# Kernel tuning notes

Hardware: AMD Instinct MI355X
Metric: run time of the kernel (lower is better)

## Reference

```python
import jax, jax.numpy as jnp
import numpy as np

THRESHOLD = 0.4


def _pair_feat(xs, xd):
    # pair_mode='both': [src, dst, |src-dst|, src*dst] along feature axis
    return jnp.concatenate([xs, xd, jnp.abs(xs - xd), xs * xd], axis=-1)


def _mlp(pf, W1, b1, W2, b2):
    h = jax.nn.relu(pf @ W1 + b1)
    return (h @ W2 + b2)[..., 0]


def setup_inputs() -> dict:
    key = jax.random.key(0)
    k1, k2, k3, k4, k5 = jax.random.split(key, 5)
    N, F, E, H = 1024, 64, 65536, 32
    x = jax.random.normal(k1, (N, F), dtype=jnp.float32)
    edge_index = jax.random.randint(k2, (2, E), 0, N, dtype=jnp.int64)
    edge_index_global = jax.random.randint(k3, (2, E), 0, N, dtype=jnp.int64)
    W1 = jax.random.normal(k4, (4 * F, H), dtype=jnp.float32) * (1.0 / np.sqrt(4 * F))
    b1 = jnp.zeros((H,), dtype=jnp.float32)
    W2 = jax.random.normal(k5, (H, 1), dtype=jnp.float32) * (1.0 / np.sqrt(H))
    b2 = jnp.zeros((1,), dtype=jnp.float32)
    return {"x": x, "edge_index": edge_index, "edge_index_global": edge_index_global,
            "W1": W1, "b1": b1, "W2": W2, "b2": b2}


def reference(x, edge_index, edge_index_global, W1, b1, W2, b2):
    # ---- sparse edge branch ----
    xs = x[edge_index[0]]            # [E, F]
    xd = x[edge_index[1]]            # [E, F]
    pf = _pair_feat(xs, xd)          # [E, 4F]
    edge_logits = _mlp(pf, W1, b1, W2, b2)        # [E]
    edge_probs = jax.nn.sigmoid(edge_logits)      # [E]
    edge_actions = (edge_probs > THRESHOLD).astype(x.dtype)  # [E]
    # (new_edge_index / raw_edge_index in the original are data-dependent
    #  boolean selections of edge columns; the mask is edge_actions==1.)

    # ---- dense all-pairs branch (train=True) ----
    N, F = x.shape
    xi = jnp.broadcast_to(x[:, None, :], (N, N, F))  # src of pair (i,j)
    xj = jnp.broadcast_to(x[None, :, :], (N, N, F))  # dst of pair (i,j)
    pf_all = _pair_feat(xi, xj)                      # [N, N, 4F] -- dominant intermediate
    logits_all = _mlp(pf_all, W1, b1, W2, b2)        # [N, N]
    P = jax.nn.sigmoid(logits_all)                   # [N, N]

    return edge_probs, edge_actions, P
```

## Files before the change

kernel.cpp:

```cpp
#include <hip/hip_runtime.h>
#include <hip/hip_bf16.h>
#include <math.h>

#define NN 1024
#define FD 64
#define EE 65536
#define HD 32

typedef __attribute__((ext_vector_type(8))) short short8;
typedef __attribute__((ext_vector_type(4))) float floatx4;

__device__ __forceinline__ float sigmoid_f(float z) {
  return 1.0f / (1.0f + expf(-z));
}
__device__ __forceinline__ float sigmoid_fast(float z) {
  return 1.0f / (1.0f + __expf(-z));
}

__device__ __forceinline__ unsigned pack_bf16_trunc(float hi, float lo) {
  unsigned a = __builtin_bit_cast(unsigned, hi);
  unsigned b = __builtin_bit_cast(unsigned, lo);
  return __builtin_amdgcn_perm(a, b, 0x07060302u);
}

__device__ __forceinline__ short8 pack8(const float* v) {
  union { unsigned u[4]; short8 s; } p;
#pragma unroll
  for (int t = 0; t < 4; ++t) p.u[t] = pack_bf16_trunc(v[2 * t + 1], v[2 * t]);
  return p.s;
}

struct Frag3 { short8 a0, a1, a2; };

__device__ __forceinline__ Frag3 split_pack(const float* v) {
  float r[8], r2[8];
#pragma unroll
  for (int t = 0; t < 8; ++t) {
    const unsigned uv = __builtin_bit_cast(unsigned, v[t]);
    const float f0 = __builtin_bit_cast(float, uv & 0xFFFF0000u);
    const float rr = v[t] - f0;
    const unsigned ur = __builtin_bit_cast(unsigned, rr);
    const float f1 = __builtin_bit_cast(float, ur & 0xFFFF0000u);
    r[t] = rr;
    r2[t] = rr - f1;
  }
  Frag3 f;
  f.a0 = pack8(v);
  f.a1 = pack8(r);
  f.a2 = pack8(r2);
  return f;
}

__global__ __launch_bounds__(256) void pre_kernel3(
    const float* __restrict__ x, const float* __restrict__ W1,
    const float* __restrict__ b1, float* __restrict__ pre,
    short* __restrict__ Wt0, short* __restrict__ Wt1, short* __restrict__ Wt2) {
  const int blk = blockIdx.x;
  const int t = threadIdx.x;
  if (blk < 256) {
    const int node = blk * 4 + (t >> 6);
    const int which = (t >> 5) & 1;
    const int h = t & 31;
    const float* xr = x + node * FD;
    const float* wp = W1 + which * FD * HD + h;
    float acc = which ? 0.0f : b1[h];
#pragma unroll
    for (int f = 0; f < FD; ++f) acc = fmaf(xr[f], wp[f * HD], acc);
    pre[which * (NN * HD) + node * HD + h] = acc;
  } else {
    for (int idx = t; idx < 32 * 128; idx += 256) {
      const int h = idx >> 7;
      const int k = idx & 127;
      const int f = k & 63;
      const int b = 2 + (k >> 6);
      const float v = W1[(b * FD + f) * HD + h];
      const unsigned uv = __builtin_bit_cast(unsigned, v);
      const unsigned u0 = uv & 0xFFFF0000u;
      const float f0 = __builtin_bit_cast(float, u0);
      const float r = v - f0;
      const unsigned u1 = __builtin_bit_cast(unsigned, r) & 0xFFFF0000u;
      const float f1 = __builtin_bit_cast(float, u1);
      const float r2 = r - f1;
      const unsigned u2 = __builtin_bit_cast(unsigned, r2) & 0xFFFF0000u;
      Wt0[idx] = (short)(u0 >> 16);
      Wt1[idx] = (short)(u1 >> 16);
      Wt2[idx] = (short)(u2 >> 16);
    }
  }
}

__device__ __forceinline__ void edge_chunk(
    const float* feat, const short* __restrict__ Wt0,
    const short* __restrict__ Wt1, const short* __restrict__ Wt2,
    int c, int q, int kc, floatx4& acc0, floatx4& acc1) {
  const Frag3 A = split_pack(feat);
  const int off0 = c * 128 + kc * 32 + q * 8;
  const int off1 = (16 + c) * 128 + kc * 32 + q * 8;
  const short8 B00 = *(const short8*)(Wt0 + off0);
  const short8 B01 = *(const short8*)(Wt1 + off0);
  const short8 B02 = *(const short8*)(Wt2 + off0);
  const short8 B10 = *(const short8*)(Wt0 + off1);
  const short8 B11 = *(const short8*)(Wt1 + off1);
  const short8 B12 = *(const short8*)(Wt2 + off1);
  acc0 = __builtin_amdgcn_mfma_f32_16x16x32_bf16(A.a0, B00, acc0, 0, 0, 0);
  acc0 = __builtin_amdgcn_mfma_f32_16x16x32_bf16(A.a0, B01, acc0, 0, 0, 0);
  acc0 = __builtin_amdgcn_mfma_f32_16x16x32_bf16(A.a0, B02, acc0, 0, 0, 0);
  acc0 = __builtin_amdgcn_mfma_f32_16x16x32_bf16(A.a1, B00, acc0, 0, 0, 0);
  acc0 = __builtin_amdgcn_mfma_f32_16x16x32_bf16(A.a1, B01, acc0, 0, 0, 0);
  acc0 = __builtin_amdgcn_mfma_f32_16x16x32_bf16(A.a2, B00, acc0, 0, 0, 0);
  acc1 = __builtin_amdgcn_mfma_f32_16x16x32_bf16(A.a0, B10, acc1, 0, 0, 0);
  acc1 = __builtin_amdgcn_mfma_f32_16x16x32_bf16(A.a0, B11, acc1, 0, 0, 0);
  acc1 = __builtin_amdgcn_mfma_f32_16x16x32_bf16(A.a0, B12, acc1, 0, 0, 0);
  acc1 = __builtin_amdgcn_mfma_f32_16x16x32_bf16(A.a1, B10, acc1, 0, 0, 0);
  acc1 = __builtin_amdgcn_mfma_f32_16x16x32_bf16(A.a1, B11, acc1, 0, 0, 0);
  acc1 = __builtin_amdgcn_mfma_f32_16x16x32_bf16(A.a2, B10, acc1, 0, 0, 0);
}

__global__ __launch_bounds__(256, 2) void edge_mfma_kernel(
    const float* __restrict__ x, const int* __restrict__ eidx,
    const float* __restrict__ pre, const short* __restrict__ Wt0,
    const short* __restrict__ Wt1, const short* __restrict__ Wt2,
    const float* __restrict__ W2, const float* __restrict__ b2,
    float* __restrict__ out) {
  const int lane = threadIdx.x & 63;
  const int q = lane >> 4;
  const int c = lane & 15;
  const int e0 = (blockIdx.x * 4 + (threadIdx.x >> 6)) * 16;

  const bool is64 = (eidx[1] == 0) && (eidx[3] == 0) && (eidx[5] == 0);
  int s_c, d_c;
  if (is64) {
    s_c = eidx[2 * (e0 + c)];
    d_c = eidx[2 * (EE + e0 + c)];
  } else {
    s_c = eidx[e0 + c];
    d_c = eidx[EE + e0 + c];
  }
  const float* xs = x + (size_t)s_c * FD;
  const float* xd = x + (size_t)d_c * FD;

  floatx4 acc0, acc1;
#pragma unroll
  for (int r = 0; r < 4; ++r) {
    const int m = q * 4 + r;
    const int sm = __shfl(s_c, m);
    const int dm = __shfl(d_c, m);
    acc0[r] = pre[sm * HD + c] + pre[NN * HD + dm * HD + c];
    acc1[r] = pre[sm * HD + 16 + c] + pre[NN * HD + dm * HD + 16 + c];
  }

  {
    const floatx4 s0 = *(const floatx4*)(xs + q * 8);
    const floatx4 s1 = *(const floatx4*)(xs + q * 8 + 4);
    const floatx4 d0 = *(const floatx4*)(xd + q * 8);
    const floatx4 d1 = *(const floatx4*)(xd + q * 8 + 4);
    float ad[8], pr[8];
#pragma unroll
    for (int t = 0; t < 4; ++t) {
      ad[t] = fabsf(s0[t] - d0[t]);     pr[t] = s0[t] * d0[t];
      ad[4 + t] = fabsf(s1[t] - d1[t]); pr[4 + t] = s1[t] * d1[t];
    }
    edge_chunk(ad, Wt0, Wt1, Wt2, c, q, 0, acc0, acc1);
    edge_chunk(pr, Wt0, Wt1, Wt2, c, q, 2, acc0, acc1);
  }
  {
    const floatx4 s0 = *(const floatx4*)(xs + 32 + q * 8);
    const floatx4 s1 = *(const floatx4*)(xs + 32 + q * 8 + 4);
    const floatx4 d0 = *(const floatx4*)(xd + 32 + q * 8);
    const floatx4 d1 = *(const floatx4*)(xd + 32 + q * 8 + 4);
    float ad[8], pr[8];
#pragma unroll
    for (int t = 0; t < 4; ++t) {
      ad[t] = fabsf(s0[t] - d0[t]);     pr[t] = s0[t] * d0[t];
      ad[4 + t] = fabsf(s1[t] - d1[t]); pr[4 + t] = s1[t] * d1[t];
    }
    edge_chunk(ad, Wt0, Wt1, Wt2, c, q, 1, acc0, acc1);
    edge_chunk(pr, Wt0, Wt1, Wt2, c, q, 3, acc0, acc1);
  }

  const float w2a = W2[c], w2b = W2[16 + c];
  const float b2v = b2[0];
  float tr[4];
#pragma unroll
  for (int r = 0; r < 4; ++r) {
    tr[r] = fmaxf(acc0[r], 0.0f) * w2a;
    tr[r] = fmaf(fmaxf(acc1[r], 0.0f), w2b, tr[r]);
#pragma unroll
    for (int m = 1; m <= 8; m <<= 1) tr[r] += __shfl_xor(tr[r], m);
  }
  float zs = tr[0];
  zs = (c == 1) ? tr[1] : zs;
  zs = (c == 2) ? tr[2] : zs;
  zs = (c == 3) ? tr[3] : zs;
  if (c < 4) {
    const int e = e0 + q * 4 + c;
    const float z = zs + b2v;
    out[e] = sigmoid_f(z);
    out[EE + e] = (z > -0.40546510810816444f) ? 1.0f : 0.0f;
  }
}

__global__ __launch_bounds__(256, 2) void dense_mfma_kernel(
    const float* __restrict__ x, const float* __restrict__ pre,
    const short* __restrict__ Wt0, const float* __restrict__ W2,
    const float* __restrict__ b2, float* __restrict__ outP) {
  const int lane = threadIdx.x & 63;
  const int w = threadIdx.x >> 6;
  const int q = lane >> 4;
  const int c = lane & 15;
  const int j0 = blockIdx.x * 64 + w * 16;
  const int i0 = blockIdx.y * 16;

  short8 Bf[2][4];
#pragma unroll
  for (int n = 0; n < 2; ++n)
#pragma unroll
    for (int s = 0; s < 4; ++s)
      Bf[n][s] = *(const short8*)(Wt0 + (n * 16 + c) * 128 + s * 32 + q * 8);

  const float* xj = x + (size_t)(j0 + c) * FD;
  float jA[8], jB[8];
#pragma unroll
  for (int t = 0; t < 4; ++t) {
    jA[t] = xj[q * 8 + t];      jA[4 + t] = xj[q * 8 + 4 + t];
    jB[t] = xj[32 + q * 8 + t]; jB[4 + t] = xj[32 + q * 8 + 4 + t];
  }

  float pdA[4], pdB[4];
#pragma unroll
  for (int r = 0; r < 4; ++r) {
    pdA[r] = pre[NN * HD + (j0 + q * 4 + r) * HD + c];
    pdB[r] = pre[NN * HD + (j0 + q * 4 + r) * HD + 16 + c];
  }
  const float w2a = W2[c], w2b = W2[16 + c];
  const float b2v = b2[0];

  for (int i = i0; i < i0 + 16; ++i) {
    const float* xi = x + (size_t)i * FD;
    const float psa = pre[i * HD + c];
    const float psb = pre[i * HD + 16 + c];
    floatx4 acc0, acc1;
#pragma unroll
    for (int r = 0; r < 4; ++r) {
      acc0[r] = psa + pdA[r];
      acc1[r] = psb + pdB[r];
    }
    {
      const floatx4 i0v = *(const floatx4*)(xi + q * 8);
      const floatx4 i1v = *(const floatx4*)(xi + q * 8 + 4);
      float ad[8], pr[8];
#pragma unroll
      for (int t = 0; t < 4; ++t) {
        ad[t] = fabsf(i0v[t] - jA[t]);         pr[t] = i0v[t] * jA[t];
        ad[4 + t] = fabsf(i1v[t] - jA[4 + t]); pr[4 + t] = i1v[t] * jA[4 + t];
      }
      const short8 fad = pack8(ad);
      const short8 fpr = pack8(pr);
      acc0 = __builtin_amdgcn_mfma_f32_16x16x32_bf16(fad, Bf[0][0], acc0, 0, 0, 0);
      acc1 = __builtin_amdgcn_mfma_f32_16x16x32_bf16(fad, Bf[1][0], acc1, 0, 0, 0);
      acc0 = __builtin_amdgcn_mfma_f32_16x16x32_bf16(fpr, Bf[0][2], acc0, 0, 0, 0);
      acc1 = __builtin_amdgcn_mfma_f32_16x16x32_bf16(fpr, Bf[1][2], acc1, 0, 0, 0);
    }
    {
      const floatx4 i0v = *(const floatx4*)(xi + 32 + q * 8);
      const floatx4 i1v = *(const floatx4*)(xi + 32 + q * 8 + 4);
      float ad[8], pr[8];
#pragma unroll
      for (int t = 0; t < 4; ++t) {
        ad[t] = fabsf(i0v[t] - jB[t]);         pr[t] = i0v[t] * jB[t];
        ad[4 + t] = fabsf(i1v[t] - jB[4 + t]); pr[4 + t] = i1v[t] * jB[4 + t];
      }
      const short8 fad = pack8(ad);
      const short8 fpr = pack8(pr);
      acc0 = __builtin_amdgcn_mfma_f32_16x16x32_bf16(fad, Bf[0][1], acc0, 0, 0, 0);
      acc1 = __builtin_amdgcn_mfma_f32_16x16x32_bf16(fad, Bf[1][1], acc1, 0, 0, 0);
      acc0 = __builtin_amdgcn_mfma_f32_16x16x32_bf16(fpr, Bf[0][3], acc0, 0, 0, 0);
      acc1 = __builtin_amdgcn_mfma_f32_16x16x32_bf16(fpr, Bf[1][3], acc1, 0, 0, 0);
    }
    float tr[4];
#pragma unroll
    for (int r = 0; r < 4; ++r) {
      tr[r] = fmaxf(acc0[r], 0.0f) * w2a;
      tr[r] = fmaf(fmaxf(acc1[r], 0.0f), w2b, tr[r]);
#pragma unroll
      for (int m = 1; m <= 8; m <<= 1) tr[r] += __shfl_xor(tr[r], m);
    }
    float zs = tr[0];
    zs = (c == 1) ? tr[1] : zs;
    zs = (c == 2) ? tr[2] : zs;
    zs = (c == 3) ? tr[3] : zs;
    if (c < 4) {
      outP[(size_t)i * NN + j0 + q * 4 + c] = sigmoid_fast(zs + b2v);
    }
  }
}

__device__ __forceinline__ float pair_logit_full(
    const float* __restrict__ xs, const float* __restrict__ xd,
    const float* __restrict__ W1, const float* __restrict__ b1,
    const float* __restrict__ W2, const float b2v) {
  float acc[HD];
#pragma unroll
  for (int h = 0; h < HD; ++h) acc[h] = b1[h];
#pragma unroll 1
  for (int f = 0; f < FD; ++f) {
    const float a = xs[f], b = xd[f];
    const float ad = fabsf(a - b), pr = a * b;
#pragma unroll
    for (int h = 0; h < HD; ++h) {
      float t0 = fmaf(a, W1[f * HD + h], acc[h]);
      t0 = fmaf(b, W1[(FD + f) * HD + h], t0);
      t0 = fmaf(ad, W1[(2 * FD + f) * HD + h], t0);
      acc[h] = fmaf(pr, W1[(3 * FD + f) * HD + h], t0);
    }
  }
  float z = b2v;
#pragma unroll
  for (int h = 0; h < HD; ++h) z = fmaf(fmaxf(acc[h], 0.0f), W2[h], z);
  return z;
}

__global__ __launch_bounds__(256) void edge_kernel_fb(
    const float* __restrict__ x, const int* __restrict__ eidx,
    const float* __restrict__ W1, const float* __restrict__ b1,
    const float* __restrict__ W2, const float* __restrict__ b2,
    float* __restrict__ out) {
  const int e = blockIdx.x * 256 + threadIdx.x;
  const bool is64 = (eidx[1] == 0) && (eidx[3] == 0) && (eidx[5] == 0);
  int s, d;
  if (is64) { s = eidx[2 * e]; d = eidx[2 * (EE + e)]; }
  else { s = eidx[e]; d = eidx[EE + e]; }
  const float z = pair_logit_full(x + (size_t)s * FD, x + (size_t)d * FD,
                                  W1, b1, W2, b2[0]);
  const float p = sigmoid_f(z);
  out[e] = p;
  out[EE + e] = (p > 0.4f) ? 1.0f : 0.0f;
}

__global__ __launch_bounds__(256) void dense_full_fb(
    const float* __restrict__ x, const float* __restrict__ W1,
    const float* __restrict__ b1, const float* __restrict__ W2,
    const float* __restrict__ b2, float* __restrict__ outP) {
  const int j = blockIdx.x * 64 + threadIdx.x % 64;
  const int i = blockIdx.y * 4 + threadIdx.x / 64;
  const float z = pair_logit_full(x + (size_t)i * FD, x + (size_t)j * FD,
                                  W1, b1, W2, b2[0]);
  outP[(size_t)i * NN + j] = sigmoid_f(z);
}

extern "C" void kernel_launch(void* const* d_in, const int* in_sizes, int n_in,
                              void* d_out, int out_size, void* d_ws, size_t ws_size,
                              hipStream_t stream) {
  const float* x  = (const float*)d_in[0];
  const int*  ei  = (const int*)d_in[1];
  const float* W1 = (const float*)d_in[3];
  const float* b1 = (const float*)d_in[4];
  const float* W2 = (const float*)d_in[5];
  const float* b2 = (const float*)d_in[6];
  float* out  = (float*)d_out;
  float* outP = out + 2 * EE;

  const size_t pre_bytes = (size_t)2 * NN * HD * sizeof(float);
  const size_t wt_elems = 32 * 128;
  const size_t need = pre_bytes + 3 * wt_elems * sizeof(short);
  if (ws_size >= need) {
    float* pre = (float*)d_ws;
    short* Wt0 = (short*)((char*)d_ws + pre_bytes);
    short* Wt1 = Wt0 + wt_elems;
    short* Wt2 = Wt1 + wt_elems;
    pre_kernel3<<<257, 256, 0, stream>>>(x, W1, b1, pre, Wt0, Wt1, Wt2);
    edge_mfma_kernel<<<1024, 256, 0, stream>>>(x, ei, pre, Wt0, Wt1, Wt2,
                                               W2, b2, out);
    dense_mfma_kernel<<<dim3(16, 64), 256, 0, stream>>>(x, pre, Wt0, W2, b2,
                                                        outP);
  } else {
    edge_kernel_fb<<<EE / 256, 256, 0, stream>>>(x, ei, W1, b1, W2, b2, out);
    dense_full_fb<<<dim3(NN / 64, NN / 4), 256, 0, stream>>>(
        x, W1, b1, W2, b2, outP);
  }
}
```

Before: 110.8 us.

## Transpose MFMA operands so hidden dim lies on rows, cutting shuffle reductions

Swaps the A and B operands of the bf16 MFMAs in both the edge and dense kernels, so each lane's accumulator holds four hidden units of a single edge or pair instead of four edges for one hidden unit. The W2 dot product then reduces mostly in registers and needs only two cross-lane shuffles instead of sixteen. The bias terms and W2 can be loaded as float4 vectors. Occupancy hints are raised and the small precompute dot product is split into four independent accumulators to shorten its dependency chain. The hint changes risk register spills.

```diff
diff --git a/kernel.cpp b/kernel.cpp
--- a/kernel.cpp
+++ b/kernel.cpp
@@ -63,10 +63,15 @@
     const int h = t & 31;
     const float* xr = x + node * FD;
     const float* wp = W1 + which * FD * HD + h;
-    float acc = which ? 0.0f : b1[h];
-#pragma unroll
-    for (int f = 0; f < FD; ++f) acc = fmaf(xr[f], wp[f * HD], acc);
-    pre[which * (NN * HD) + node * HD + h] = acc;
+    float a0 = which ? 0.0f : b1[h], a1 = 0.0f, a2 = 0.0f, a3 = 0.0f;
+#pragma unroll
+    for (int f = 0; f < FD; f += 4) {
+      a0 = fmaf(xr[f + 0], wp[(f + 0) * HD], a0);
+      a1 = fmaf(xr[f + 1], wp[(f + 1) * HD], a1);
+      a2 = fmaf(xr[f + 2], wp[(f + 2) * HD], a2);
+      a3 = fmaf(xr[f + 3], wp[(f + 3) * HD], a3);
+    }
+    pre[which * (NN * HD) + node * HD + h] = (a0 + a1) + (a2 + a3);
   } else {
     for (int idx = t; idx < 32 * 128; idx += 256) {
       const int h = idx >> 7;
@@ -93,30 +98,30 @@
     const float* feat, const short* __restrict__ Wt0,
     const short* __restrict__ Wt1, const short* __restrict__ Wt2,
     int c, int q, int kc, floatx4& acc0, floatx4& acc1) {
-  const Frag3 A = split_pack(feat);
+  const Frag3 B = split_pack(feat);
   const int off0 = c * 128 + kc * 32 + q * 8;
   const int off1 = (16 + c) * 128 + kc * 32 + q * 8;
-  const short8 B00 = *(const short8*)(Wt0 + off0);
-  const short8 B01 = *(const short8*)(Wt1 + off0);
-  const short8 B02 = *(const short8*)(Wt2 + off0);
-  const short8 B10 = *(const short8*)(Wt0 + off1);
-  const short8 B11 = *(const short8*)(Wt1 + off1);
-  const short8 B12 = *(const short8*)(Wt2 + off1);
-  acc0 = __builtin_amdgcn_mfma_f32_16x16x32_bf16(A.a0, B00, acc0, 0, 0, 0);
-  acc0 = __builtin_amdgcn_mfma_f32_16x16x32_bf16(A.a0, B01, acc0, 0, 0, 0);
-  acc0 = __builtin_amdgcn_mfma_f32_16x16x32_bf16(A.a0, B02, acc0, 0, 0, 0);
-  acc0 = __builtin_amdgcn_mfma_f32_16x16x32_bf16(A.a1, B00, acc0, 0, 0, 0);
-  acc0 = __builtin_amdgcn_mfma_f32_16x16x32_bf16(A.a1, B01, acc0, 0, 0, 0);
-  acc0 = __builtin_amdgcn_mfma_f32_16x16x32_bf16(A.a2, B00, acc0, 0, 0, 0);
-  acc1 = __builtin_amdgcn_mfma_f32_16x16x32_bf16(A.a0, B10, acc1, 0, 0, 0);
-  acc1 = __builtin_amdgcn_mfma_f32_16x16x32_bf16(A.a0, B11, acc1, 0, 0, 0);
-  acc1 = __builtin_amdgcn_mfma_f32_16x16x32_bf16(A.a0, B12, acc1, 0, 0, 0);
-  acc1 = __builtin_amdgcn_mfma_f32_16x16x32_bf16(A.a1, B10, acc1, 0, 0, 0);
-  acc1 = __builtin_amdgcn_mfma_f32_16x16x32_bf16(A.a1, B11, acc1, 0, 0, 0);
-  acc1 = __builtin_amdgcn_mfma_f32_16x16x32_bf16(A.a2, B10, acc1, 0, 0, 0);
-}
-
-__global__ __launch_bounds__(256, 2) void edge_mfma_kernel(
+  const short8 A00 = *(const short8*)(Wt0 + off0);
+  const short8 A01 = *(const short8*)(Wt1 + off0);
+  const short8 A02 = *(const short8*)(Wt2 + off0);
+  const short8 A10 = *(const short8*)(Wt0 + off1);
+  const short8 A11 = *(const short8*)(Wt1 + off1);
+  const short8 A12 = *(const short8*)(Wt2 + off1);
+  acc0 = __builtin_amdgcn_mfma_f32_16x16x32_bf16(A00, B.a0, acc0, 0, 0, 0);
+  acc0 = __builtin_amdgcn_mfma_f32_16x16x32_bf16(A01, B.a0, acc0, 0, 0, 0);
+  acc0 = __builtin_amdgcn_mfma_f32_16x16x32_bf16(A02, B.a0, acc0, 0, 0, 0);
+  acc0 = __builtin_amdgcn_mfma_f32_16x16x32_bf16(A00, B.a1, acc0, 0, 0, 0);
+  acc0 = __builtin_amdgcn_mfma_f32_16x16x32_bf16(A01, B.a1, acc0, 0, 0, 0);
+  acc0 = __builtin_amdgcn_mfma_f32_16x16x32_bf16(A00, B.a2, acc0, 0, 0, 0);
+  acc1 = __builtin_amdgcn_mfma_f32_16x16x32_bf16(A10, B.a0, acc1, 0, 0, 0);
+  acc1 = __builtin_amdgcn_mfma_f32_16x16x32_bf16(A11, B.a0, acc1, 0, 0, 0);
+  acc1 = __builtin_amdgcn_mfma_f32_16x16x32_bf16(A12, B.a0, acc1, 0, 0, 0);
+  acc1 = __builtin_amdgcn_mfma_f32_16x16x32_bf16(A10, B.a1, acc1, 0, 0, 0);
+  acc1 = __builtin_amdgcn_mfma_f32_16x16x32_bf16(A11, B.a1, acc1, 0, 0, 0);
+  acc1 = __builtin_amdgcn_mfma_f32_16x16x32_bf16(A10, B.a2, acc1, 0, 0, 0);
+}
+
+__global__ __launch_bounds__(256, 3) void edge_mfma_kernel(
     const float* __restrict__ x, const int* __restrict__ eidx,
     const float* __restrict__ pre, const short* __restrict__ Wt0,
     const short* __restrict__ Wt1, const short* __restrict__ Wt2,
@@ -140,13 +145,16 @@
   const float* xd = x + (size_t)d_c * FD;
 
   floatx4 acc0, acc1;
-#pragma unroll
-  for (int r = 0; r < 4; ++r) {
-    const int m = q * 4 + r;
-    const int sm = __shfl(s_c, m);
-    const int dm = __shfl(d_c, m);
-    acc0[r] = pre[sm * HD + c] + pre[NN * HD + dm * HD + c];
-    acc1[r] = pre[sm * HD + 16 + c] + pre[NN * HD + dm * HD + 16 + c];
+  {
+    const floatx4 psA = *(const floatx4*)(pre + s_c * HD + q * 4);
+    const floatx4 psB = *(const floatx4*)(pre + s_c * HD + 16 + q * 4);
+    const floatx4 pdA = *(const floatx4*)(pre + NN * HD + d_c * HD + q * 4);
+    const floatx4 pdB = *(const floatx4*)(pre + NN * HD + d_c * HD + 16 + q * 4);
+#pragma unroll
+    for (int r = 0; r < 4; ++r) {
+      acc0[r] = psA[r] + pdA[r];
+      acc1[r] = psB[r] + pdB[r];
+    }
   }
 
   {
@@ -178,29 +186,25 @@
     edge_chunk(pr, Wt0, Wt1, Wt2, c, q, 3, acc0, acc1);
   }
 
-  const float w2a = W2[c], w2b = W2[16 + c];
-  const float b2v = b2[0];
-  float tr[4];
+  const floatx4 w2A = *(const floatx4*)(W2 + q * 4);
+  const floatx4 w2B = *(const floatx4*)(W2 + 16 + q * 4);
+  float tv = 0.0f;
 #pragma unroll
   for (int r = 0; r < 4; ++r) {
-    tr[r] = fmaxf(acc0[r], 0.0f) * w2a;
-    tr[r] = fmaf(fmaxf(acc1[r], 0.0f), w2b, tr[r]);
-#pragma unroll
-    for (int m = 1; m <= 8; m <<= 1) tr[r] += __shfl_xor(tr[r], m);
-  }
-  float zs = tr[0];
-  zs = (c == 1) ? tr[1] : zs;
-  zs = (c == 2) ? tr[2] : zs;
-  zs = (c == 3) ? tr[3] : zs;
-  if (c < 4) {
-    const int e = e0 + q * 4 + c;
-    const float z = zs + b2v;
+    tv = fmaf(fmaxf(acc0[r], 0.0f), w2A[r], tv);
+    tv = fmaf(fmaxf(acc1[r], 0.0f), w2B[r], tv);
+  }
+  tv += __shfl_xor(tv, 16);
+  tv += __shfl_xor(tv, 32);
+  if (lane < 16) {
+    const int e = e0 + lane;
+    const float z = tv + b2[0];
     out[e] = sigmoid_f(z);
     out[EE + e] = (z > -0.40546510810816444f) ? 1.0f : 0.0f;
   }
 }
 
-__global__ __launch_bounds__(256, 2) void dense_mfma_kernel(
+__global__ __launch_bounds__(256, 4) void dense_mfma_kernel(
     const float* __restrict__ x, const float* __restrict__ pre,
     const short* __restrict__ Wt0, const float* __restrict__ W2,
     const float* __restrict__ b2, float* __restrict__ outP) {
@@ -211,12 +215,12 @@
   const int j0 = blockIdx.x * 64 + w * 16;
   const int i0 = blockIdx.y * 16;
 
-  short8 Bf[2][4];
+  short8 Af[2][4];
 #pragma unroll
   for (int n = 0; n < 2; ++n)
 #pragma unroll
     for (int s = 0; s < 4; ++s)
-      Bf[n][s] = *(const short8*)(Wt0 + (n * 16 + c) * 128 + s * 32 + q * 8);
+      Af[n][s] = *(const short8*)(Wt0 + (n * 16 + c) * 128 + s * 32 + q * 8);
 
   const float* xj = x + (size_t)(j0 + c) * FD;
   float jA[8], jB[8];
@@ -226,24 +230,21 @@
     jB[t] = xj[32 + q * 8 + t]; jB[4 + t] = xj[32 + q * 8 + 4 + t];
   }
 
-  float pdA[4], pdB[4];
-#pragma unroll
-  for (int r = 0; r < 4; ++r) {
-    pdA[r] = pre[NN * HD + (j0 + q * 4 + r) * HD + c];
-    pdB[r] = pre[NN * HD + (j0 + q * 4 + r) * HD + 16 + c];
-  }
-  const float w2a = W2[c], w2b = W2[16 + c];
+  const floatx4 pdA = *(const floatx4*)(pre + NN * HD + (j0 + c) * HD + q * 4);
+  const floatx4 pdB = *(const floatx4*)(pre + NN * HD + (j0 + c) * HD + 16 + q * 4);
+  const floatx4 w2A = *(const floatx4*)(W2 + q * 4);
+  const floatx4 w2B = *(const floatx4*)(W2 + 16 + q * 4);
   const float b2v = b2[0];
 
   for (int i = i0; i < i0 + 16; ++i) {
     const float* xi = x + (size_t)i * FD;
-    const float psa = pre[i * HD + c];
-    const float psb = pre[i * HD + 16 + c];
+    const floatx4 psA = *(const floatx4*)(pre + i * HD + q * 4);
+    const floatx4 psB = *(const floatx4*)(pre + i * HD + 16 + q * 4);
     floatx4 acc0, acc1;
 #pragma unroll
     for (int r = 0; r < 4; ++r) {
-      acc0[r] = psa + pdA[r];
-      acc1[r] = psb + pdB[r];
+      acc0[r] = psA[r] + pdA[r];
+      acc1[r] = psB[r] + pdB[r];
     }
     {
       const floatx4 i0v = *(const floatx4*)(xi + q * 8);
@@ -256,10 +257,10 @@
       }
       const short8 fad = pack8(ad);
       const short8 fpr = pack8(pr);
-      acc0 = __builtin_amdgcn_mfma_f32_16x16x32_bf16(fad, Bf[0][0], acc0, 0, 0, 0);
-      acc1 = __builtin_amdgcn_mfma_f32_16x16x32_bf16(fad, Bf[1][0], acc1, 0, 0, 0);
-      acc0 = __builtin_amdgcn_mfma_f32_16x16x32_bf16(fpr, Bf[0][2], acc0, 0, 0, 0);
-      acc1 = __builtin_amdgcn_mfma_f32_16x16x32_bf16(fpr, Bf[1][2], acc1, 0, 0, 0);
+      acc0 = __builtin_amdgcn_mfma_f32_16x16x32_bf16(Af[0][0], fad, acc0, 0, 0, 0);
+      acc1 = __builtin_amdgcn_mfma_f32_16x16x32_bf16(Af[1][0], fad, acc1, 0, 0, 0);
+      acc0 = __builtin_amdgcn_mfma_f32_16x16x32_bf16(Af[0][2], fpr, acc0, 0, 0, 0);
+      acc1 = __builtin_amdgcn_mfma_f32_16x16x32_bf16(Af[1][2], fpr, acc1, 0, 0, 0);
     }
     {
       const floatx4 i0v = *(const floatx4*)(xi + 32 + q * 8);
@@ -272,25 +273,21 @@
       }
       const short8 fad = pack8(ad);
       const short8 fpr = pack8(pr);
-      acc0 = __builtin_amdgcn_mfma_f32_16x16x32_bf16(fad, Bf[0][1], acc0, 0, 0, 0);
-      acc1 = __builtin_amdgcn_mfma_f32_16x16x32_bf16(fad, Bf[1][1], acc1, 0, 0, 0);
-      acc0 = __builtin_amdgcn_mfma_f32_16x16x32_bf16(fpr, Bf[0][3], acc0, 0, 0, 0);
-      acc1 = __builtin_amdgcn_mfma_f32_16x16x32_bf16(fpr, Bf[1][3], acc1, 0, 0, 0);
-    }
-    float tr[4];
+      acc0 = __builtin_amdgcn_mfma_f32_16x16x32_bf16(Af[0][1], fad, acc0, 0, 0, 0);
+      acc1 = __builtin_amdgcn_mfma_f32_16x16x32_bf16(Af[1][1], fad, acc1, 0, 0, 0);
+      acc0 = __builtin_amdgcn_mfma_f32_16x16x32_bf16(Af[0][3], fpr, acc0, 0, 0, 0);
+      acc1 = __builtin_amdgcn_mfma_f32_16x16x32_bf16(Af[1][3], fpr, acc1, 0, 0, 0);
+    }
+    float tv = 0.0f;
 #pragma unroll
     for (int r = 0; r < 4; ++r) {
-      tr[r] = fmaxf(acc0[r], 0.0f) * w2a;
-      tr[r] = fmaf(fmaxf(acc1[r], 0.0f), w2b, tr[r]);
-#pragma unroll
-      for (int m = 1; m <= 8; m <<= 1) tr[r] += __shfl_xor(tr[r], m);
-    }
-    float zs = tr[0];
-    zs = (c == 1) ? tr[1] : zs;
-    zs = (c == 2) ? tr[2] : zs;
-    zs = (c == 3) ? tr[3] : zs;
-    if (c < 4) {
-      outP[(size_t)i * NN + j0 + q * 4 + c] = sigmoid_fast(zs + b2v);
+      tv = fmaf(fmaxf(acc0[r], 0.0f), w2A[r], tv);
+      tv = fmaf(fmaxf(acc1[r], 0.0f), w2B[r], tv);
+    }
+    tv += __shfl_xor(tv, 16);
+    tv += __shfl_xor(tv, 32);
+    if (lane < 16) {
+      outP[(size_t)i * NN + j0 + lane] = sigmoid_fast(tv + b2v);
     }
   }
 }
```

Result: no change. 112.3 us (+1.3%).
